# Kernel optimization log

Hardware: AMD Instinct MI355X
Metric: run time of the kernel (lower is better)

Reference implementation:

```python
import jax, jax.numpy as jnp
import numpy as np
from jax import lax

D_CONV = 4


def setup_inputs() -> dict:
    key = jax.random.key(0)
    ks = jax.random.split(key, 8)
    b, L, d_model = 2, 1024, 1024
    d_inner, d_state = 2048, 16
    s = 0.02  # weight scale
    return {
        "x": jax.random.normal(ks[0], (b, L, d_model), jnp.float32),
        "in_w": jax.random.normal(ks[1], (2 * d_inner, d_model), jnp.float32) * s,
        "in_b": jnp.zeros((2 * d_inner,), jnp.float32),
        "conv_w": jax.random.normal(ks[2], (d_inner, 1, D_CONV), jnp.float32) * s,
        "conv_b": jnp.zeros((d_inner,), jnp.float32),
        "xproj_w": jax.random.normal(ks[3], (2 * d_state + 1, d_inner), jnp.float32) * s,
        "dt_w": jax.random.normal(ks[4], (d_inner, 1), jnp.float32) * s,
        "dt_b": jnp.zeros((d_inner,), jnp.float32),
        "A_log": jax.random.normal(ks[5], (d_inner, d_state), jnp.float32),
        "D": jnp.ones((d_inner,), jnp.float32),
        "out_w": jax.random.normal(ks[6], (d_model, d_inner), jnp.float32) * s,
    }


def reference(x, in_w, in_b, conv_w, conv_b, xproj_w, dt_w, dt_b, A_log, D, out_w):
    b, L, _ = x.shape
    d_inner = conv_w.shape[0]
    d_state = A_log.shape[1]

    xz = x @ in_w.T + in_b                       # (b, L, 2*d_inner)
    xh, z = jnp.split(xz, 2, axis=-1)            # each (b, L, d_inner)

    # depthwise causal conv1d (torch pads d_conv-1 both sides then slices [:L])
    xc = jnp.transpose(xh, (0, 2, 1))            # (b, d_inner, L)
    xc = lax.conv_general_dilated(
        xc, conv_w, window_strides=(1,), padding=[(D_CONV - 1, 0)],
        feature_group_count=d_inner, dimension_numbers=("NCH", "OIH", "NCH"))
    xc = xc + conv_b[None, :, None]
    xh = jnp.transpose(xc, (0, 2, 1))            # (b, L, d_inner)

    xh = xh * jax.nn.silu(z)

    proj = xh @ xproj_w.T                        # (b, L, 2*d_state+1)
    dlt = proj[..., :1]                          # (b, L, 1)
    B = proj[..., 1:1 + d_state]                 # (b, L, d_state)
    C = proj[..., 1 + d_state:]                  # (b, L, d_state)

    # dt_proj: (b,L,1) -> (b,L,d_inner); source applies softplus then exp
    delta = jnp.exp(jax.nn.softplus(dlt @ dt_w.T + dt_b))  # (b, L, d_inner)

    A = -jnp.exp(A_log)                          # (d_inner, d_state)

    def step(h, inp):
        xt, dt, Bt, Ct = inp                     # (b,i), (b,i), (b,s), (b,s)
        A_bar = jnp.exp(A[None] * dt[..., None])          # (b, i, s)
        B_bar = dt[..., None] * Bt[:, None, :]            # (b, i, s)
        h = A_bar * h + B_bar * xt[..., None]             # (b, i, s)
        yt = jnp.einsum("bis,bs->bi", h, Ct)              # (b, i)
        return h, yt

    h0 = jnp.zeros((b, d_inner, d_state), x.dtype)
    xs = (jnp.moveaxis(xh, 1, 0), jnp.moveaxis(delta, 1, 0),
          jnp.moveaxis(B, 1, 0), jnp.moveaxis(C, 1, 0))
    _, ys = lax.scan(step, h0, xs)               # (L, b, d_inner)
    y = jnp.moveaxis(ys, 0, 1) + D * xh          # (b, L, d_inner)

    return y @ out_w.T                           # (b, L, d_model)
```

## Files before the change

### kernel.cpp

```cpp
#include <hip/hip_runtime.h>
#include <hip/hip_bf16.h>

#define NTOK   2048
#define DMODEL 1024
#define DINNER 2048
#define DSTATE 16
#define SEQLEN 1024
#define NPROJ  33
#define NPAD   48
#define CCH    64
#define CT     16

typedef __attribute__((ext_vector_type(8))) short bf16x8;
typedef __attribute__((ext_vector_type(4))) float f32x4;
typedef __attribute__((ext_vector_type(8))) unsigned short us8;

__device__ __forceinline__ unsigned short f2bf(float f) {
  unsigned u = __float_as_uint(f);
  return (unsigned short)((u + 0x7FFFu + ((u >> 16) & 1u)) >> 16);
}
__device__ __forceinline__ float bf2f(unsigned short u) {
  return __uint_as_float(((unsigned)u) << 16);
}

__device__ __forceinline__ void gload_lds16(const void* g, void* l) {
  __builtin_amdgcn_global_load_lds(
      (const __attribute__((address_space(1))) unsigned int*)g,
      (__attribute__((address_space(3))) unsigned int*)l, 16, 0, 0);
}

#define CAST_N0 (NTOK * DMODEL)
#define CAST_N1 (CAST_N0 + 2 * DINNER * DMODEL)
#define CAST_N2 (CAST_N1 + NPAD * DINNER)
__global__ __launch_bounds__(256) void cast3_bf16_kernel(
    const float* __restrict__ s0, const float* __restrict__ s1,
    const float* __restrict__ s3, unsigned short* __restrict__ dst,
    float* __restrict__ proj) {
  if (blockIdx.x < 33) {
    const int o = blockIdx.x * 2048 + threadIdx.x * 8;
    const float4 z4 = make_float4(0.f, 0.f, 0.f, 0.f);
    *(float4*)(proj + o) = z4;
    *(float4*)(proj + o + 4) = z4;
  }
  const int idx = (blockIdx.x * 256 + threadIdx.x) * 8;
  const float* src;
  int off;
  if (idx < CAST_N0) { src = s0; off = idx; }
  else if (idx < CAST_N1) { src = s1; off = idx - CAST_N0; }
  else {
    off = idx - CAST_N1;
    if (off >= NPROJ * DINNER) {
      us8 z = {0, 0, 0, 0, 0, 0, 0, 0};
      *(us8*)(dst + idx) = z;
      return;
    }
    src = s3;
  }
  const float4 a = *(const float4*)(src + off);
  const float4 b = *(const float4*)(src + off + 4);
  us8 o;
  o[0] = f2bf(a.x); o[1] = f2bf(a.y); o[2] = f2bf(a.z); o[3] = f2bf(a.w);
  o[4] = f2bf(b.x); o[5] = f2bf(b.y); o[6] = f2bf(b.z); o[7] = f2bf(b.w);
  *(us8*)(dst + idx) = o;
}

__global__ __launch_bounds__(256) void gemm_bt_mfma(
    const unsigned short* __restrict__ A, const unsigned short* __restrict__ B,
    const float* __restrict__ bias, unsigned short* __restrict__ C,
    int M, int K) {
  constexpr int BN = 128, TN = 4;
  __shared__ unsigned short As[2][128 * 32];
  __shared__ unsigned short Bs[2][BN * 32];

  const int tid = threadIdx.x;
  const int wid = tid >> 6;
  const int lane = tid & 63;
  const int n0 = blockIdx.x * 128;
  const int m0 = blockIdx.y * BN;

  const int wave_m = wid & 1;
  const int wave_n = wid >> 1;
  const int lm = lane & 15;
  const int lq = lane >> 4;

  f32x4 acc[4][TN] = {};

  for (int k0 = 0; k0 < K; k0 += 64) {
    __syncthreads();
#pragma unroll
    for (int h = 0; h < 2; ++h) {
      const int kh = k0 + h * 32;
#pragma unroll
      for (int j = 0; j < 2; ++j) {
        const int cb = j * 256 + wid * 64;
        const int c = cb + lane;
        gload_lds16(A + (size_t)(n0 + (c >> 2)) * K + kh + (c & 3) * 8,
                    &As[h][cb * 8]);
      }
#pragma unroll
      for (int j = 0; j < BN / 64; ++j) {
        const int cb = j * 256 + wid * 64;
        const int c = cb + lane;
        gload_lds16(B + (size_t)(m0 + (c >> 2)) * K + kh + (c & 3) * 8,
                    &Bs[h][cb * 8]);
      }
    }
    __syncthreads();

#pragma unroll
    for (int h = 0; h < 2; ++h) {
      bf16x8 af[4], bfr[TN];
#pragma unroll
      for (int tm = 0; tm < 4; ++tm)
        af[tm] = *(const bf16x8*)
            &As[h][(wave_m * 64 + tm * 16 + lm) * 32 + lq * 8];
#pragma unroll
      for (int tn = 0; tn < TN; ++tn)
        bfr[tn] = *(const bf16x8*)
            &Bs[h][(wave_n * (BN / 2) + tn * 16 + lm) * 32 + lq * 8];
#pragma unroll
      for (int tm = 0; tm < 4; ++tm)
#pragma unroll
        for (int tn = 0; tn < TN; ++tn)
          acc[tm][tn] = __builtin_amdgcn_mfma_f32_16x16x32_bf16(
              af[tm], bfr[tn], acc[tm][tn], 0, 0, 0);
    }
  }

#pragma unroll
  for (int tm = 0; tm < 4; ++tm) {
    const int row = n0 + wave_m * 64 + tm * 16 + lq * 4;
#pragma unroll
    for (int tn = 0; tn < TN; ++tn) {
      const int col = m0 + wave_n * (BN / 2) + tn * 16 + lm;
      const float bv = bias[col];
#pragma unroll
      for (int r = 0; r < 4; ++r)
        C[(size_t)(row + r) * M + col] = f2bf(acc[tm][tn][r] + bv);
    }
  }
}

__global__ __launch_bounds__(256) void gemm_bt_mfma_sk(
    const unsigned short* __restrict__ A, const unsigned short* __restrict__ B,
    float* __restrict__ C, int M, int K) {
  constexpr int BN = 64, TN = 2;
  __shared__ unsigned short As[2][128 * 32];
  __shared__ unsigned short Bs[2][BN * 32];

  const int tid = threadIdx.x;
  const int wid = tid >> 6;
  const int lane = tid & 63;
  const int n0 = blockIdx.x * 128;
  const int m0 = blockIdx.y * BN;
  const int kstart = blockIdx.z * (K >> 1);

  const int wave_m = wid & 1;
  const int wave_n = wid >> 1;
  const int lm = lane & 15;
  const int lq = lane >> 4;

  f32x4 acc[4][TN] = {};

  for (int k0 = kstart; k0 < kstart + (K >> 1); k0 += 64) {
    __syncthreads();
#pragma unroll
    for (int h = 0; h < 2; ++h) {
      const int kh = k0 + h * 32;
#pragma unroll
      for (int j = 0; j < 2; ++j) {
        const int cb = j * 256 + wid * 64;
        const int c = cb + lane;
        gload_lds16(A + (size_t)(n0 + (c >> 2)) * K + kh + (c & 3) * 8,
                    &As[h][cb * 8]);
      }
      {
        const int cb = wid * 64;
        const int c = cb + lane;
        gload_lds16(B + (size_t)(m0 + (c >> 2)) * K + kh + (c & 3) * 8,
                    &Bs[h][cb * 8]);
      }
    }
    __syncthreads();

#pragma unroll
    for (int h = 0; h < 2; ++h) {
      bf16x8 af[4], bfr[TN];
#pragma unroll
      for (int tm = 0; tm < 4; ++tm)
        af[tm] = *(const bf16x8*)
            &As[h][(wave_m * 64 + tm * 16 + lm) * 32 + lq * 8];
#pragma unroll
      for (int tn = 0; tn < TN; ++tn)
        bfr[tn] = *(const bf16x8*)
            &Bs[h][(wave_n * (BN / 2) + tn * 16 + lm) * 32 + lq * 8];
#pragma unroll
      for (int tm = 0; tm < 4; ++tm)
#pragma unroll
        for (int tn = 0; tn < TN; ++tn)
          acc[tm][tn] = __builtin_amdgcn_mfma_f32_16x16x32_bf16(
              af[tm], bfr[tn], acc[tm][tn], 0, 0, 0);
    }
  }

#pragma unroll
  for (int tm = 0; tm < 4; ++tm) {
    const int row = n0 + wave_m * 64 + tm * 16 + lq * 4;
#pragma unroll
    for (int tn = 0; tn < TN; ++tn) {
      const int col = m0 + wave_n * (BN / 2) + tn * 16 + lm;
#pragma unroll
      for (int r = 0; r < 4; ++r)
        atomicAdd(&C[(size_t)(row + r) * M + col], acc[tm][tn][r]);
    }
  }
}

__global__ __launch_bounds__(256) void conv_xproj_mfma(
    const unsigned short* __restrict__ xz, const float* __restrict__ cw,
    const float* __restrict__ cb, const unsigned short* __restrict__ wp,
    float* __restrict__ xg, float* __restrict__ proj) {
  __shared__ unsigned short As[4][64 * 32];
  __shared__ unsigned short Bs[4][NPAD * 32];

  const int tid = threadIdx.x;
  const int wid = tid >> 6;
  const int lane = tid & 63;
  const int n0 = blockIdx.x * 64;
  const int kb = blockIdx.y * 128;

#pragma unroll
  for (int j = 0; j < 3; ++j) {
    const int cbase = j * 256 + wid * 64;
    const int c = cbase + lane;
    const int stage = c / 192;
    const int rem = c - stage * 192;
    gload_lds16(wp + (size_t)(rem >> 2) * DINNER + kb + stage * 32 + (rem & 3) * 8,
                &Bs[0][0] + cbase * 8);
  }

  const int c128 = tid & 127;
  const int half = tid >> 7;
  const int i = kb + c128;
  const int gt0 = n0 + half * 32;
  const float4 w4 = ((const float4*)cw)[i];
  const float cbv = cb[i];

  const bool seq_start = ((gt0 & (SEQLEN - 1)) == 0);
  float tm3 = seq_start ? 0.f : bf2f(xz[(size_t)(gt0 - 3) * (2 * DINNER) + i]);
  float tm2 = seq_start ? 0.f : bf2f(xz[(size_t)(gt0 - 2) * (2 * DINNER) + i]);
  float tm1 = seq_start ? 0.f : bf2f(xz[(size_t)(gt0 - 1) * (2 * DINNER) + i]);

  unsigned short* Arow = &As[c128 >> 5][c128 & 31];
#pragma unroll 4
  for (int t = 0; t < 32; ++t) {
    const int n = gt0 + t;
    const float x0 = bf2f(xz[(size_t)n * (2 * DINNER) + i]);
    float acc = cbv;
    acc = fmaf(w4.x, tm3, acc);
    acc = fmaf(w4.y, tm2, acc);
    acc = fmaf(w4.z, tm1, acc);
    acc = fmaf(w4.w, x0, acc);
    const float z = bf2f(xz[(size_t)n * (2 * DINNER) + DINNER + i]);
    const float sig = 1.f / (1.f + __expf(-z));
    const float v = acc * (z * sig);
    xg[(size_t)n * DINNER + i] = v;
    Arow[(half * 32 + t) * 32] = f2bf(v);
    tm3 = tm2; tm2 = tm1; tm1 = x0;
  }
  __syncthreads();

  const int lm = lane & 15;
  const int lq = lane >> 4;
  f32x4 acc[3] = {};
#pragma unroll
  for (int stage = 0; stage < 4; ++stage) {
    bf16x8 af = *(const bf16x8*)&As[stage][(wid * 16 + lm) * 32 + lq * 8];
#pragma unroll
    for (int tn = 0; tn < 3; ++tn) {
      bf16x8 bfr = *(const bf16x8*)&Bs[stage][(tn * 16 + lm) * 32 + lq * 8];
      acc[tn] = __builtin_amdgcn_mfma_f32_16x16x32_bf16(af, bfr, acc[tn], 0, 0, 0);
    }
  }

  const int row = n0 + wid * 16 + lq * 4;
#pragma unroll
  for (int tn = 0; tn < 3; ++tn) {
    const int col = tn * 16 + lm;
    if (col < NPROJ) {
#pragma unroll
      for (int r = 0; r < 4; ++r)
        atomicAdd(&proj[(size_t)(row + r) * NPROJ + col], acc[tn][r]);
    }
  }
}

__global__ __launch_bounds__(256) void scan_phase1(
    const float* __restrict__ xg, const float* __restrict__ proj,
    const float* __restrict__ dt_w, const float* __restrict__ dt_b,
    const float* __restrict__ A_log,
    float* __restrict__ Sbuf, float* __restrict__ Hbuf) {
  __shared__ float pl[CT][36];
  const int tid = threadIdx.x;
  const int i = blockIdx.x * 256 + tid;
  const int k = blockIdx.y;
  const int b = blockIdx.z;
  const int n0 = b * SEQLEN + k * CT;

  for (int e = tid; e < CT * NPROJ; e += 256) {
    const int t = e / NPROJ;
    const int c = e - t * NPROJ;
    pl[t][c] = proj[(size_t)(n0 + t) * NPROJ + c];
  }
  __syncthreads();

  const float dtw = dt_w[i], dtb = dt_b[i];
  float Av[DSTATE];
#pragma unroll
  for (int s = 0; s < DSTATE; ++s) Av[s] = -__expf(A_log[i * DSTATE + s]);

  float h[DSTATE] = {};
  float Ssum = 0.f;

  for (int t = 0; t < CT; ++t) {
    const float delta = 1.f + __expf(fmaf(pl[t][0], dtw, dtb));
    Ssum += delta;
    const float x = xg[(size_t)(n0 + t) * DINNER + i];
    const float dx = delta * x;
#pragma unroll
    for (int s = 0; s < DSTATE; ++s)
      h[s] = fmaf(__expf(Av[s] * delta), h[s], pl[t][1 + s] * dx);
  }

  const size_t ck = (size_t)(b * CCH + k) * DINNER + i;
  Sbuf[ck] = Ssum;
  float4* Hq = (float4*)(Hbuf + ck * DSTATE);
#pragma unroll
  for (int q = 0; q < 4; ++q)
    Hq[q] = make_float4(h[4 * q], h[4 * q + 1], h[4 * q + 2], h[4 * q + 3]);
}

__global__ __launch_bounds__(256) void scan_phase2(
    const float* __restrict__ A_log, const float* __restrict__ Sbuf,
    float* __restrict__ Hbuf, float* __restrict__ out,
    const float* __restrict__ out_w, unsigned short* __restrict__ outw_bf) {
  const int gid = blockIdx.x * 256 + threadIdx.x;
  const float4 z4 = make_float4(0.f, 0.f, 0.f, 0.f);
#pragma unroll
  for (int j = 0; j < 8; ++j)
    *(float4*)(out + (size_t)(j * 65536 + gid) * 4) = z4;

  {
    const int base = gid * 32;
#pragma unroll
    for (int q = 0; q < 4; ++q) {
      const float4 a = *(const float4*)(out_w + base + q * 8);
      const float4 b = *(const float4*)(out_w + base + q * 8 + 4);
      us8 o;
      o[0] = f2bf(a.x); o[1] = f2bf(a.y); o[2] = f2bf(a.z); o[3] = f2bf(a.w);
      o[4] = f2bf(b.x); o[5] = f2bf(b.y); o[6] = f2bf(b.z); o[7] = f2bf(b.w);
      *(us8*)(outw_bf + base + q * 8) = o;
    }
  }

  const int s = gid & (DSTATE - 1);
  const int i = (gid >> 4) & (DINNER - 1);
  const int b = gid >> 15;
  const float Av = -__expf(A_log[i * DSTATE + s]);
  float H = 0.f;
  for (int k = 0; k < CCH; ++k) {
    const size_t ck = (size_t)(b * CCH + k) * DINNER + i;
    const float hk = Hbuf[ck * DSTATE + s];
    const float a = __expf(Av * Sbuf[ck]);
    Hbuf[ck * DSTATE + s] = H;
    H = fmaf(a, H, hk);
  }
}

__global__ __launch_bounds__(256) void scan_phase3(
    const float* __restrict__ xg, const float* __restrict__ proj,
    const float* __restrict__ dt_w, const float* __restrict__ dt_b,
    const float* __restrict__ A_log, const float* __restrict__ Dp,
    const float* __restrict__ Hbuf, unsigned short* __restrict__ y) {
  __shared__ float pl[CT][36];
  const int tid = threadIdx.x;
  const int i = blockIdx.x * 256 + tid;
  const int k = blockIdx.y;
  const int b = blockIdx.z;
  const int n0 = b * SEQLEN + k * CT;

  for (int e = tid; e < CT * NPROJ; e += 256) {
    const int t = e / NPROJ;
    const int c = e - t * NPROJ;
    pl[t][c] = proj[(size_t)(n0 + t) * NPROJ + c];
  }
  __syncthreads();

  const float dtw = dt_w[i], dtb = dt_b[i];
  const float Dv = Dp[i];
  float Av[DSTATE];
#pragma unroll
  for (int s = 0; s < DSTATE; ++s) Av[s] = -__expf(A_log[i * DSTATE + s]);

  const size_t ck = (size_t)(b * CCH + k) * DINNER + i;
  float h[DSTATE];
  const float4* Hq = (const float4*)(Hbuf + ck * DSTATE);
#pragma unroll
  for (int q = 0; q < 4; ++q) {
    const float4 v = Hq[q];
    h[4 * q + 0] = v.x; h[4 * q + 1] = v.y;
    h[4 * q + 2] = v.z; h[4 * q + 3] = v.w;
  }

  for (int t = 0; t < CT; ++t) {
    const float delta = 1.f + __expf(fmaf(pl[t][0], dtw, dtb));
    const float x = xg[(size_t)(n0 + t) * DINNER + i];
    const float dx = delta * x;
    float yt = 0.f;
#pragma unroll
    for (int s = 0; s < DSTATE; ++s) {
      h[s] = fmaf(__expf(Av[s] * delta), h[s], pl[t][1 + s] * dx);
      yt = fmaf(h[s], pl[t][17 + s], yt);
    }
    y[(size_t)(n0 + t) * DINNER + i] = f2bf(fmaf(Dv, x, yt));
  }
}

extern "C" void kernel_launch(void* const* d_in, const int* in_sizes, int n_in,
                              void* d_out, int out_size, void* d_ws, size_t ws_size,
                              hipStream_t stream) {
  const float* x       = (const float*)d_in[0];
  const float* in_w    = (const float*)d_in[1];
  const float* in_b    = (const float*)d_in[2];
  const float* conv_w  = (const float*)d_in[3];
  const float* conv_b  = (const float*)d_in[4];
  const float* xproj_w = (const float*)d_in[5];
  const float* dt_w    = (const float*)d_in[6];
  const float* dt_b    = (const float*)d_in[7];
  const float* A_log   = (const float*)d_in[8];
  const float* Dp      = (const float*)d_in[9];
  const float* out_w   = (const float*)d_in[10];
  float* out = (float*)d_out;

  float* ws = (float*)d_ws;
  unsigned short* xz_bf = (unsigned short*)ws;
  float* xg = ws + 8388608;
  unsigned short* bf_base = (unsigned short*)(ws + 12582912);
  unsigned short* x_bf    = bf_base;
  unsigned short* inw_bf  = bf_base + CAST_N0;
  unsigned short* wpad_bf = bf_base + CAST_N1;
  unsigned short* outw_bf = bf_base + CAST_N2;
  unsigned short* yb_bf = (unsigned short*)(ws + 16826368);
  float* proj = ws + 18923520;
  float* Sbuf = ws + 19005440;
  float* Hbuf = ws + 19267584;

  cast3_bf16_kernel<<<CAST_N2 / (256 * 8), 256, 0, stream>>>(
      x, in_w, xproj_w, bf_base, proj);

  gemm_bt_mfma<<<dim3(NTOK / 128, (2 * DINNER) / 128), 256, 0, stream>>>(
      x_bf, inw_bf, in_b, xz_bf, 2 * DINNER, DMODEL);

  conv_xproj_mfma<<<dim3(NTOK / 64, DINNER / 128), 256, 0, stream>>>(
      xz_bf, conv_w, conv_b, wpad_bf, xg, proj);

  scan_phase1<<<dim3(DINNER / 256, CCH, 2), 256, 0, stream>>>(
      xg, proj, dt_w, dt_b, A_log, Sbuf, Hbuf);
  scan_phase2<<<(2 * DINNER * DSTATE) / 256, 256, 0, stream>>>(
      A_log, Sbuf, Hbuf, out, out_w, outw_bf);
  scan_phase3<<<dim3(DINNER / 256, CCH, 2), 256, 0, stream>>>(
      xg, proj, dt_w, dt_b, A_log, Dp, Hbuf, yb_bf);

  gemm_bt_mfma_sk<<<dim3(NTOK / 128, DMODEL / 64, 2), 256, 0, stream>>>(
      yb_bf, outw_bf, out, DMODEL, DINNER);
}
```

Before: 213.5 us.

## Fuse three chunked scan phases into one kernel with LDS carry propagation

Replaces the three scan kernels (chunk-local scan, cross-chunk carry, chunk rescan) with one kernel in which each block owns 4 channels across all 64 chunks. Chunk summaries stay in shared memory and the carry pass runs on 64 threads, while the other threads zero the output and cast out_w to bf16. The proj buffer is padded to a stride of 36 so rows can be read with float4 loads straight from global memory instead of being staged in LDS. This removes two kernel launches and the Hbuf/Sbuf round trips through global memory. In exchange, the xg accesses now come from only 4 adjacent channels per token row, so they are poorly coalesced, and most threads sit idle during the serial carry pass.

```diff
diff --git a/kernel.cpp b/kernel.cpp
--- a/kernel.cpp
+++ b/kernel.cpp
@@ -8,6 +8,7 @@
 #define SEQLEN 1024
 #define NPROJ  33
 #define NPAD   48
+#define PSTRIDE 36
 #define CCH    64
 #define CT     16
 
@@ -36,7 +37,7 @@
     const float* __restrict__ s0, const float* __restrict__ s1,
     const float* __restrict__ s3, unsigned short* __restrict__ dst,
     float* __restrict__ proj) {
-  if (blockIdx.x < 33) {
+  if (blockIdx.x < 36) {
     const int o = blockIdx.x * 2048 + threadIdx.x * 8;
     const float4 z4 = make_float4(0.f, 0.f, 0.f, 0.f);
     *(float4*)(proj + o) = z4;
@@ -290,29 +291,26 @@
     if (col < NPROJ) {
 #pragma unroll
       for (int r = 0; r < 4; ++r)
-        atomicAdd(&proj[(size_t)(row + r) * NPROJ + col], acc[tn][r]);
-    }
-  }
-}
-
-__global__ __launch_bounds__(256) void scan_phase1(
+        atomicAdd(&proj[(size_t)(row + r) * PSTRIDE + col], acc[tn][r]);
+    }
+  }
+}
+
+__global__ __launch_bounds__(256) void scan_fused(
     const float* __restrict__ xg, const float* __restrict__ proj,
     const float* __restrict__ dt_w, const float* __restrict__ dt_b,
-    const float* __restrict__ A_log,
-    float* __restrict__ Sbuf, float* __restrict__ Hbuf) {
-  __shared__ float pl[CT][36];
+    const float* __restrict__ A_log, const float* __restrict__ Dp,
+    float* __restrict__ out, const float* __restrict__ out_w,
+    unsigned short* __restrict__ outw_bf, unsigned short* __restrict__ y) {
+  __shared__ float Hl[4][CCH][DSTATE];
+  __shared__ float Sl[4][CCH];
+
   const int tid = threadIdx.x;
-  const int i = blockIdx.x * 256 + tid;
-  const int k = blockIdx.y;
-  const int b = blockIdx.z;
+  const int c = tid & 3;
+  const int k = tid >> 2;
+  const int b = blockIdx.y;
+  const int i = blockIdx.x * 4 + c;
   const int n0 = b * SEQLEN + k * CT;
-
-  for (int e = tid; e < CT * NPROJ; e += 256) {
-    const int t = e / NPROJ;
-    const int c = e - t * NPROJ;
-    pl[t][c] = proj[(size_t)(n0 + t) * NPROJ + c];
-  }
-  __syncthreads();
 
   const float dtw = dt_w[i], dtb = dt_b[i];
   float Av[DSTATE];
@@ -321,106 +319,76 @@
 
   float h[DSTATE] = {};
   float Ssum = 0.f;
-
   for (int t = 0; t < CT; ++t) {
-    const float delta = 1.f + __expf(fmaf(pl[t][0], dtw, dtb));
+    const float* pr = proj + (size_t)(n0 + t) * PSTRIDE;
+    float fr[20];
+#pragma unroll
+    for (int j = 0; j < 5; ++j) {
+      const float4 v = *(const float4*)(pr + j * 4);
+      fr[4 * j + 0] = v.x; fr[4 * j + 1] = v.y;
+      fr[4 * j + 2] = v.z; fr[4 * j + 3] = v.w;
+    }
+    const float delta = 1.f + __expf(fmaf(fr[0], dtw, dtb));
     Ssum += delta;
     const float x = xg[(size_t)(n0 + t) * DINNER + i];
     const float dx = delta * x;
 #pragma unroll
     for (int s = 0; s < DSTATE; ++s)
-      h[s] = fmaf(__expf(Av[s] * delta), h[s], pl[t][1 + s] * dx);
-  }
-
-  const size_t ck = (size_t)(b * CCH + k) * DINNER + i;
-  Sbuf[ck] = Ssum;
-  float4* Hq = (float4*)(Hbuf + ck * DSTATE);
-#pragma unroll
-  for (int q = 0; q < 4; ++q)
-    Hq[q] = make_float4(h[4 * q], h[4 * q + 1], h[4 * q + 2], h[4 * q + 3]);
-}
-
-__global__ __launch_bounds__(256) void scan_phase2(
-    const float* __restrict__ A_log, const float* __restrict__ Sbuf,
-    float* __restrict__ Hbuf, float* __restrict__ out,
-    const float* __restrict__ out_w, unsigned short* __restrict__ outw_bf) {
-  const int gid = blockIdx.x * 256 + threadIdx.x;
-  const float4 z4 = make_float4(0.f, 0.f, 0.f, 0.f);
-#pragma unroll
-  for (int j = 0; j < 8; ++j)
-    *(float4*)(out + (size_t)(j * 65536 + gid) * 4) = z4;
-
-  {
-    const int base = gid * 32;
-#pragma unroll
-    for (int q = 0; q < 4; ++q) {
-      const float4 a = *(const float4*)(out_w + base + q * 8);
-      const float4 b = *(const float4*)(out_w + base + q * 8 + 4);
+      h[s] = fmaf(__expf(Av[s] * delta), h[s], fr[1 + s] * dx);
+  }
+  Sl[c][k] = Ssum;
+#pragma unroll
+  for (int s = 0; s < DSTATE; ++s) Hl[c][k][s] = h[s];
+  __syncthreads();
+
+  if (tid < 64) {
+    const int cc = tid & 3;
+    const int s = tid >> 2;
+    const float Av2 = -__expf(A_log[(blockIdx.x * 4 + cc) * DSTATE + s]);
+    float H = 0.f;
+#pragma unroll 4
+    for (int k2 = 0; k2 < CCH; ++k2) {
+      const float hk = Hl[cc][k2][s];
+      const float a = __expf(Av2 * Sl[cc][k2]);
+      Hl[cc][k2][s] = H;
+      H = fmaf(a, H, hk);
+    }
+  } else {
+    const int gid = (b * 512 + blockIdx.x) * 192 + (tid - 64);
+    const float4 z4 = make_float4(0.f, 0.f, 0.f, 0.f);
+    for (int j = gid; j < (NTOK * DMODEL) / 4; j += 196608)
+      ((float4*)out)[j] = z4;
+    for (int j = gid; j < (DMODEL * DINNER) / 8; j += 196608) {
+      const float4 a = *(const float4*)(out_w + j * 8);
+      const float4 bq = *(const float4*)(out_w + j * 8 + 4);
       us8 o;
       o[0] = f2bf(a.x); o[1] = f2bf(a.y); o[2] = f2bf(a.z); o[3] = f2bf(a.w);
-      o[4] = f2bf(b.x); o[5] = f2bf(b.y); o[6] = f2bf(b.z); o[7] = f2bf(b.w);
-      *(us8*)(outw_bf + base + q * 8) = o;
-    }
-  }
-
-  const int s = gid & (DSTATE - 1);
-  const int i = (gid >> 4) & (DINNER - 1);
-  const int b = gid >> 15;
-  const float Av = -__expf(A_log[i * DSTATE + s]);
-  float H = 0.f;
-  for (int k = 0; k < CCH; ++k) {
-    const size_t ck = (size_t)(b * CCH + k) * DINNER + i;
-    const float hk = Hbuf[ck * DSTATE + s];
-    const float a = __expf(Av * Sbuf[ck]);
-    Hbuf[ck * DSTATE + s] = H;
-    H = fmaf(a, H, hk);
-  }
-}
-
-__global__ __launch_bounds__(256) void scan_phase3(
-    const float* __restrict__ xg, const float* __restrict__ proj,
-    const float* __restrict__ dt_w, const float* __restrict__ dt_b,
-    const float* __restrict__ A_log, const float* __restrict__ Dp,
-    const float* __restrict__ Hbuf, unsigned short* __restrict__ y) {
-  __shared__ float pl[CT][36];
-  const int tid = threadIdx.x;
-  const int i = blockIdx.x * 256 + tid;
-  const int k = blockIdx.y;
-  const int b = blockIdx.z;
-  const int n0 = b * SEQLEN + k * CT;
-
-  for (int e = tid; e < CT * NPROJ; e += 256) {
-    const int t = e / NPROJ;
-    const int c = e - t * NPROJ;
-    pl[t][c] = proj[(size_t)(n0 + t) * NPROJ + c];
+      o[4] = f2bf(bq.x); o[5] = f2bf(bq.y); o[6] = f2bf(bq.z); o[7] = f2bf(bq.w);
+      *(us8*)(outw_bf + j * 8) = o;
+    }
   }
   __syncthreads();
 
-  const float dtw = dt_w[i], dtb = dt_b[i];
   const float Dv = Dp[i];
-  float Av[DSTATE];
-#pragma unroll
-  for (int s = 0; s < DSTATE; ++s) Av[s] = -__expf(A_log[i * DSTATE + s]);
-
-  const size_t ck = (size_t)(b * CCH + k) * DINNER + i;
-  float h[DSTATE];
-  const float4* Hq = (const float4*)(Hbuf + ck * DSTATE);
-#pragma unroll
-  for (int q = 0; q < 4; ++q) {
-    const float4 v = Hq[q];
-    h[4 * q + 0] = v.x; h[4 * q + 1] = v.y;
-    h[4 * q + 2] = v.z; h[4 * q + 3] = v.w;
-  }
-
+#pragma unroll
+  for (int s = 0; s < DSTATE; ++s) h[s] = Hl[c][k][s];
   for (int t = 0; t < CT; ++t) {
-    const float delta = 1.f + __expf(fmaf(pl[t][0], dtw, dtb));
+    const float* pr = proj + (size_t)(n0 + t) * PSTRIDE;
+    float fr[36];
+#pragma unroll
+    for (int j = 0; j < 9; ++j) {
+      const float4 v = *(const float4*)(pr + j * 4);
+      fr[4 * j + 0] = v.x; fr[4 * j + 1] = v.y;
+      fr[4 * j + 2] = v.z; fr[4 * j + 3] = v.w;
+    }
+    const float delta = 1.f + __expf(fmaf(fr[0], dtw, dtb));
     const float x = xg[(size_t)(n0 + t) * DINNER + i];
     const float dx = delta * x;
     float yt = 0.f;
 #pragma unroll
     for (int s = 0; s < DSTATE; ++s) {
-      h[s] = fmaf(__expf(Av[s] * delta), h[s], pl[t][1 + s] * dx);
-      yt = fmaf(h[s], pl[t][17 + s], yt);
+      h[s] = fmaf(__expf(Av[s] * delta), h[s], fr[1 + s] * dx);
+      yt = fmaf(h[s], fr[17 + s], yt);
     }
     y[(size_t)(n0 + t) * DINNER + i] = f2bf(fmaf(Dv, x, yt));
   }
@@ -452,8 +420,6 @@
   unsigned short* outw_bf = bf_base + CAST_N2;
   unsigned short* yb_bf = (unsigned short*)(ws + 16826368);
   float* proj = ws + 18923520;
-  float* Sbuf = ws + 19005440;
-  float* Hbuf = ws + 19267584;
 
   cast3_bf16_kernel<<<CAST_N2 / (256 * 8), 256, 0, stream>>>(
       x, in_w, xproj_w, bf_base, proj);
@@ -464,12 +430,8 @@
   conv_xproj_mfma<<<dim3(NTOK / 64, DINNER / 128), 256, 0, stream>>>(
       xz_bf, conv_w, conv_b, wpad_bf, xg, proj);
 
-  scan_phase1<<<dim3(DINNER / 256, CCH, 2), 256, 0, stream>>>(
-      xg, proj, dt_w, dt_b, A_log, Sbuf, Hbuf);
-  scan_phase2<<<(2 * DINNER * DSTATE) / 256, 256, 0, stream>>>(
-      A_log, Sbuf, Hbuf, out, out_w, outw_bf);
-  scan_phase3<<<dim3(DINNER / 256, CCH, 2), 256, 0, stream>>>(
-      xg, proj, dt_w, dt_b, A_log, Dp, Hbuf, yb_bf);
+  scan_fused<<<dim3(DINNER / 4, 2), 256, 0, stream>>>(
+      xg, proj, dt_w, dt_b, A_log, Dp, out, out_w, outw_bf, yb_bf);
 
   gemm_bt_mfma_sk<<<dim3(NTOK / 128, DMODEL / 64, 2), 256, 0, stream>>>(
       yb_bf, outw_bf, out, DMODEL, DINNER);
```

Result: slower. 222.4 us (+4.2%).
